# Kernel optimization log

Measured on AMD Instinct MI355X. Metric: run time of the kernel, lower is better.

Reference implementation:

```python
import jax, jax.numpy as jnp
import numpy as np

N = 256
DT = 1.0 / 4096.0
BATCH = 256
LENGTH = 4096

def _legt_transition(n):
    # HiPPO-LegT continuous-time transition (Gu et al.)
    Q = np.arange(n, dtype=np.float64)
    R = (2.0 * Q + 1.0) ** 0.5
    j, i = np.meshgrid(Q, Q)
    A = R[:, None] * np.where(i < j, (-1.0) ** (i - j), 1.0) * R[None, :]
    B = R[:, None]
    return -A, B

def _bilinear(A, B, dt):
    # scipy cont2discrete(method='bilinear'), alpha=0.5
    n = A.shape[0]
    ima = np.eye(n) - 0.5 * dt * A
    Ad = np.linalg.solve(ima, np.eye(n) + 0.5 * dt * A)
    Bd = np.linalg.solve(ima, dt * B)
    return Ad, Bd

def setup_inputs() -> dict:
    key = jax.random.key(0)
    Ac, Bc = _legt_transition(N)
    evals = (2.0 * np.arange(N, dtype=np.float64) + 1.0) ** 0.5
    C = evals @ Ac                        # (N,) readout from continuous A
    D = np.sum(evals * Bc.squeeze(-1))    # scalar
    scale = 1.0 / (1.0 - 0.5 * D * DT)
    C_discr = (scale * 0.5 * DT * C).astype(np.float32)          # (N,)
    D_discr = np.array([scale * (1.0 + 0.5 * DT * D)], np.float32)  # (1,)
    Ad, Bd = _bilinear(Ac, Bc, DT)
    inputs = jax.random.normal(key, (BATCH, LENGTH), dtype=jnp.float32)
    return {
        "inputs": inputs,
        "A": jnp.asarray(Ad, dtype=jnp.float32),
        "B": jnp.asarray(Bd.squeeze(-1), dtype=jnp.float32),
        "C_discr": jnp.asarray(C_discr),
        "D_discr": jnp.asarray(D_discr),
    }

def reference(inputs, A, B, C_discr, D_discr):
    # inputs: (batch, length). teacher_ratio=1.0 -> fully teacher-forced LTI scan:
    #   c_t = A c_{t-1} + B * u_t ;  pred_t = fac_t * (c_t @ C) + D * u_t
    # where fac_0 = 1 and fac_t = 2 for t > 0 (as in the torch loop).
    batch, length = inputs.shape
    c0 = jnp.zeros((batch, A.shape[0]), dtype=inputs.dtype)
    facs = jnp.where(jnp.arange(length) == 0, 1.0, 2.0).astype(inputs.dtype)

    def step(c, xs):
        x_t, fac = xs                                   # x_t: (batch,)
        c = c @ A.T + B[None, :] * x_t[:, None]         # (batch, N); F.linear(c, A)
        pred = fac * (c @ C_discr) + D_discr[0] * x_t   # (batch,)
        return c, pred

    _, preds = jax.lax.scan(step, c0, (inputs.T, facs))  # preds: (length, batch)
    return preds.T  # (batch, length)
```

## Files before the change

kernel.cpp:

```cpp
#include <hip/hip_runtime.h>


#define LENGTH 4096

#define WS_P2    0
#define WS_P4    65536
#define WS_P8    131072
#define WS_P16   196608
#define WS_P32   262144
#define WS_P64T  327680
#define WS_P128T 393216
#define WS_W     458752
#define WS_V     475136
#define WS_K     491520
#define WS_XH    495616
#define WS_XL    1019904
#define WS_AH    1544192
#define WS_AL    1609728

typedef __attribute__((ext_vector_type(8))) short bf16x8;
typedef __attribute__((ext_vector_type(4))) float f32x4;
#define MFMA(a, b, c) __builtin_amdgcn_mfma_f32_16x16x32_bf16(a, b, c, 0, 0, 0)

__device__ inline unsigned short f2bf(float f) {
    unsigned int u = __float_as_uint(f);
    return (unsigned short)((u + 0x7FFFu + ((u >> 16) & 1u)) >> 16);
}
__device__ inline void split2(float f, short& h, short& l) {
    unsigned short hu = f2bf(f);
    float fh = __uint_as_float((unsigned int)hu << 16);
    h = (short)hu;
    l = (short)f2bf(f - fh);
}

__global__ __launch_bounds__(1024) void mmrow(const float* __restrict__ X,
                                              const float* __restrict__ Y,
                                              float* __restrict__ Z) {
    const int i = blockIdx.x, t = threadIdx.x;
    const int j = t & 255, p = t >> 8;
    __shared__ float red[3][256];
    const float* xr = X + i * 256 + 64 * p;
    const float* yc = Y + (64 * p) * 256 + j;
    float a0 = 0.f, a1 = 0.f, a2 = 0.f, a3 = 0.f;
#pragma unroll
    for (int l = 0; l < 64; l += 4) {
        a0 = fmaf(xr[l + 0], yc[(l + 0) * 256], a0);
        a1 = fmaf(xr[l + 1], yc[(l + 1) * 256], a1);
        a2 = fmaf(xr[l + 2], yc[(l + 2) * 256], a2);
        a3 = fmaf(xr[l + 3], yc[(l + 3) * 256], a3);
    }
    float s = (a0 + a1) + (a2 + a3);
    if (p) red[p - 1][j] = s;
    __syncthreads();
    if (p == 0) Z[i * 256 + j] = s + red[0][j] + red[1][j] + red[2][j];
}

__global__ __launch_bounds__(1024) void mm2(const float* __restrict__ P32,
                                            float* __restrict__ P64T) {
    const int i = blockIdx.x, t = threadIdx.x;
    const int j = t & 255, p = t >> 8;
    __shared__ float red[3][256];
    const float* xr = P32 + i * 256 + 64 * p;
    const float* yc = P32 + (64 * p) * 256 + j;
    float a0 = 0.f, a1 = 0.f, a2 = 0.f, a3 = 0.f;
#pragma unroll
    for (int l = 0; l < 64; l += 4) {
        a0 = fmaf(xr[l + 0], yc[(l + 0) * 256], a0);
        a1 = fmaf(xr[l + 1], yc[(l + 1) * 256], a1);
        a2 = fmaf(xr[l + 2], yc[(l + 2) * 256], a2);
        a3 = fmaf(xr[l + 3], yc[(l + 3) * 256], a3);
    }
    float s = (a0 + a1) + (a2 + a3);
    if (p) red[p - 1][j] = s;
    __syncthreads();
    if (p == 0) P64T[j * 256 + i] = s + red[0][j] + red[1][j] + red[2][j];
}

__global__ __launch_bounds__(1024) void wvgen(const float* __restrict__ A,
                                              const float* __restrict__ B,
                                              const float* __restrict__ C,
                                              const float* __restrict__ P32,
                                              const float* __restrict__ P64T,
                                              const float* __restrict__ P128T,
                                              float* __restrict__ W,
                                              float* __restrict__ V) {
    const int t = threadIdx.x;
    const int bid = blockIdx.x;
    const int j = t & 255, p = t >> 8;
    __shared__ float cur[256];
    __shared__ float red[4][256];

    if (bid < 2) {
        float areg[64];
#pragma unroll
        for (int ii = 0; ii < 64; ++ii) areg[ii] = A[(64 * p + ii) * 256 + j];

        if (bid == 0) {
            if (t < 256) cur[t] = C[t];
            __syncthreads();
        } else {
            float s0 = 0.f, s1 = 0.f, s2 = 0.f, s3 = 0.f;
#pragma unroll 4
            for (int ii = 0; ii < 64; ii += 4) {
                s0 = fmaf(C[64 * p + ii + 0], P32[(64 * p + ii + 0) * 256 + j], s0);
                s1 = fmaf(C[64 * p + ii + 1], P32[(64 * p + ii + 1) * 256 + j], s1);
                s2 = fmaf(C[64 * p + ii + 2], P32[(64 * p + ii + 2) * 256 + j], s2);
                s3 = fmaf(C[64 * p + ii + 3], P32[(64 * p + ii + 3) * 256 + j], s3);
            }
            red[p][j] = (s0 + s1) + (s2 + s3);
            __syncthreads();
            if (p == 0) cur[j] = red[0][j] + red[1][j] + red[2][j] + red[3][j];
            __syncthreads();
        }
        const int base = bid * 32;
        if (p == 0) W[base * 256 + j] = cur[j];
        for (int r = 1; r < 32; ++r) {
            float s0 = 0.f, s1 = 0.f, s2 = 0.f, s3 = 0.f;
#pragma unroll
            for (int m = 0; m < 16; ++m) {
                float4 c4 = *reinterpret_cast<const float4*>(&cur[64 * p + 4 * m]);
                s0 = fmaf(c4.x, areg[4 * m + 0], s0);
                s1 = fmaf(c4.y, areg[4 * m + 1], s1);
                s2 = fmaf(c4.z, areg[4 * m + 2], s2);
                s3 = fmaf(c4.w, areg[4 * m + 3], s3);
            }
            red[p][j] = (s0 + s1) + (s2 + s3);
            __syncthreads();
            if (p == 0) {
                float s = red[0][j] + red[1][j] + red[2][j] + red[3][j];
                cur[j] = s;
                W[(base + r) * 256 + j] = s;
            }
            __syncthreads();
        }
    } else {
        const int i = j;
        float mreg[64];
#pragma unroll
        for (int jj = 0; jj < 64; ++jj) mreg[jj] = P128T[(64 * p + jj) * 256 + i];
        if (t < 256) cur[t] = B[t];
        __syncthreads();

        if (bid == 3) {
            float s0 = 0.f, s1 = 0.f, s2 = 0.f, s3 = 0.f;
#pragma unroll 4
            for (int jj = 0; jj < 64; jj += 4) {
                s0 = fmaf(P64T[(64 * p + jj + 0) * 256 + i], cur[64 * p + jj + 0], s0);
                s1 = fmaf(P64T[(64 * p + jj + 1) * 256 + i], cur[64 * p + jj + 1], s1);
                s2 = fmaf(P64T[(64 * p + jj + 2) * 256 + i], cur[64 * p + jj + 2], s2);
                s3 = fmaf(P64T[(64 * p + jj + 3) * 256 + i], cur[64 * p + jj + 3], s3);
            }
            red[p][i] = (s0 + s1) + (s2 + s3);
            __syncthreads();
            if (p == 0) cur[i] = red[0][i] + red[1][i] + red[2][i] + red[3][i];
            __syncthreads();
        }
        const int off = bid - 2;
        for (int m = 0; m < 32; ++m) {
            if (p == 0) V[(2 * m + off) * 256 + i] = cur[i];
            if (m == 31) break;
            float s0 = 0.f, s1 = 0.f, s2 = 0.f, s3 = 0.f;
#pragma unroll
            for (int mm = 0; mm < 16; ++mm) {
                float4 c4 = *reinterpret_cast<const float4*>(&cur[64 * p + 4 * mm]);
                s0 = fmaf(c4.x, mreg[4 * mm + 0], s0);
                s1 = fmaf(c4.y, mreg[4 * mm + 1], s1);
                s2 = fmaf(c4.z, mreg[4 * mm + 2], s2);
                s3 = fmaf(c4.w, mreg[4 * mm + 3], s3);
            }
            red[p][i] = (s0 + s1) + (s2 + s3);
            __syncthreads();
            if (p == 0) cur[i] = red[0][i] + red[1][i] + red[2][i] + red[3][i];
            __syncthreads();
        }
    }
}

__global__ __launch_bounds__(256) void kdot(const float* __restrict__ W,
                                            const float* __restrict__ V,
                                            float* __restrict__ K) {
    const int q = blockIdx.x, tid = threadIdx.x;
    const int r = tid & 63, p = tid >> 6;
    __shared__ float Wl[64 * 257];
    __shared__ float Vl[256];
    __shared__ float red[4][64];
    for (int u = 0; u < 64; ++u) Wl[u * 257 + tid] = W[u * 256 + tid];
    Vl[tid] = V[q * 256 + tid];
    __syncthreads();
    float s0 = 0.f, s1 = 0.f;
#pragma unroll
    for (int m = 0; m < 64; m += 2) {
        s0 = fmaf(Wl[r * 257 + 64 * p + m + 0], Vl[64 * p + m + 0], s0);
        s1 = fmaf(Wl[r * 257 + 64 * p + m + 1], Vl[64 * p + m + 1], s1);
    }
    red[p][r] = s0 + s1;
    __syncthreads();
    if (tid < 64) K[q * 64 + tid] = red[0][tid] + red[1][tid] + red[2][tid] + red[3][tid];
}

__global__ __launch_bounds__(256) void xsplit(const float* __restrict__ x,
                                              short* __restrict__ XH,
                                              short* __restrict__ XL) {
    const int w = threadIdx.x >> 6, lane = threadIdx.x & 63;
    const int p = blockIdx.x * 4 + w;
    const int c = p >> 4, blk = p & 15;
    const int b = blk * 16 + (lane & 15);
    const int s0 = c * 32 + 8 * (lane >> 4);
    const float4 v0 = reinterpret_cast<const float4*>(&x[b * LENGTH + s0])[0];
    const float4 v1 = reinterpret_cast<const float4*>(&x[b * LENGTH + s0])[1];
    const float f[8] = {v0.x, v0.y, v0.z, v0.w, v1.x, v1.y, v1.z, v1.w};
    bf16x8 hv, lv;
#pragma unroll
    for (int e = 0; e < 8; ++e) {
        short h, l;
        split2(f[e], h, l);
        hv[e] = h; lv[e] = l;
    }
    const int off = (p * 64 + lane) * 8;
    *reinterpret_cast<bf16x8*>(XH + off) = hv;
    *reinterpret_cast<bf16x8*>(XL + off) = lv;
}

__global__ __launch_bounds__(256) void afrag(const float* __restrict__ K,
                                             short* __restrict__ AH,
                                             short* __restrict__ AL) {
    const int m = blockIdx.x * 4 + (threadIdx.x >> 6);
    const int lane = threadIdx.x & 63;
    bf16x8 hv, lv;
#pragma unroll
    for (int e = 0; e < 8; ++e) {
        const int kidx = 16 * m + (lane & 15) - 8 * (lane >> 4) - e;
        const float kv = (kidx >= 0) ? K[kidx] : 0.f;
        short h, l;
        split2(kv, h, l);
        hv[e] = h; lv[e] = l;
    }
    const int off = (m * 64 + lane) * 8;
    *reinterpret_cast<bf16x8*>(AH + off) = hv;
    *reinterpret_cast<bf16x8*>(AL + off) = lv;
}

struct Frag {
    bf16x8 bh0, bh1, bl0, bl1;
    bf16x8 ah0, ah1, ah2, ah3, al0, al1, al2, al3;
    int d0, tile;
};

__global__ __launch_bounds__(512) void convm(const short* __restrict__ XH,
                                             const short* __restrict__ XL,
                                             const short* __restrict__ AH,
                                             const short* __restrict__ AL,
                                             const float* __restrict__ x,
                                             const float* __restrict__ Dp,
                                             float* __restrict__ out) {
    const int pr = blockIdx.x & 31;
    const int bt = blockIdx.x >> 5;
    const int tid = threadIdx.x;
    const int w = tid >> 6, lane = tid & 63;
    const int tA64 = pr * 64, tB64 = (63 - pr) * 64;
    const int nA = 2 * pr + 2;
    const int bt2 = bt * 2;

    __shared__ float lds[16 * 64 * 34];

    f32x4 acc[2][4][2];
#pragma unroll
    for (int t_ = 0; t_ < 2; ++t_)
#pragma unroll
        for (int r_ = 0; r_ < 4; ++r_)
#pragma unroll
            for (int c_ = 0; c_ < 2; ++c_) acc[t_][r_][c_] = f32x4{0.f, 0.f, 0.f, 0.f};

#define LOADF(F, IDX_) do {                                                    \
        const int i_ = (IDX_);                                                 \
        const int tl_ = (i_ < nA) ? 0 : 1;                                     \
        const int cc_ = i_ - (tl_ ? nA : 0);                                   \
        const int xo_ = ((cc_ * 16 + bt2) * 64 + lane) * 8;                    \
        F.bh0 = *reinterpret_cast<const bf16x8*>(XH + xo_);                    \
        F.bh1 = *reinterpret_cast<const bf16x8*>(XH + xo_ + 512);              \
        F.bl0 = *reinterpret_cast<const bf16x8*>(XL + xo_);                    \
        F.bl1 = *reinterpret_cast<const bf16x8*>(XL + xo_ + 512);              \
        const int d_ = (tl_ ? tB64 : tA64) - cc_ * 32;                         \
        F.d0 = d_; F.tile = tl_;                                               \
        const int m0_ = (d_ > 0 ? d_ : 0) >> 4;                                \
        const int m1_ = (d_ + 16 > 0 ? d_ + 16 : 0) >> 4;                      \
        const int m2_ = (d_ + 32 > 0 ? d_ + 32 : 0) >> 4;                      \
        const int m3_ = (d_ + 48 > 0 ? d_ + 48 : 0) >> 4;                      \
        F.ah0 = *reinterpret_cast<const bf16x8*>(AH + (m0_ * 64 + lane) * 8);  \
        F.al0 = *reinterpret_cast<const bf16x8*>(AL + (m0_ * 64 + lane) * 8);  \
        F.ah1 = *reinterpret_cast<const bf16x8*>(AH + (m1_ * 64 + lane) * 8);  \
        F.al1 = *reinterpret_cast<const bf16x8*>(AL + (m1_ * 64 + lane) * 8);  \
        F.ah2 = *reinterpret_cast<const bf16x8*>(AH + (m2_ * 64 + lane) * 8);  \
        F.al2 = *reinterpret_cast<const bf16x8*>(AL + (m2_ * 64 + lane) * 8);  \
        F.ah3 = *reinterpret_cast<const bf16x8*>(AH + (m3_ * 64 + lane) * 8);  \
        F.al3 = *reinterpret_cast<const bf16x8*>(AL + (m3_ * 64 + lane) * 8);  \
    } while (0)

#define ONER(F, T, R, AHF, ALF)                                                \
        if (F.d0 + 16 * R >= 0) {                                              \
            acc[T][R][0] = MFMA(F.AHF, F.bh0, acc[T][R][0]);                   \
            acc[T][R][1] = MFMA(F.AHF, F.bh1, acc[T][R][1]);                   \
            acc[T][R][0] = MFMA(F.AHF, F.bl0, acc[T][R][0]);                   \
            acc[T][R][1] = MFMA(F.AHF, F.bl1, acc[T][R][1]);                   \
            acc[T][R][0] = MFMA(F.ALF, F.bh0, acc[T][R][0]);                   \
            acc[T][R][1] = MFMA(F.ALF, F.bh1, acc[T][R][1]);                   \
        }

#define APPLY(F) do {                                                          \
        if (F.tile == 0) {                                                     \
            ONER(F, 0, 0, ah0, al0) ONER(F, 0, 1, ah1, al1)                    \
            ONER(F, 0, 2, ah2, al2) ONER(F, 0, 3, ah3, al3)                    \
        } else {                                                               \
            ONER(F, 1, 0, ah0, al0) ONER(F, 1, 1, ah1, al1)                    \
            ONER(F, 1, 2, ah2, al2) ONER(F, 1, 3, ah3, al3)                    \
        }                                                                      \
    } while (0)

    Frag f0, f1;
    LOADF(f0, w);
    int idx = w;
    while (true) {
        const int n1 = idx + 8;
        const bool h1 = n1 < 130;
        if (h1) LOADF(f1, n1);
        APPLY(f0);
        if (!h1) break;
        const int n2 = n1 + 8;
        const bool h2 = n2 < 130;
        if (h2) LOADF(f0, n2);
        APPLY(f1);
        if (!h2) break;
        idx = n2;
    }

    const int lq = lane >> 4, lr = lane & 15;
#pragma unroll
    for (int t_ = 0; t_ < 2; ++t_)
#pragma unroll
        for (int r_ = 0; r_ < 4; ++r_)
#pragma unroll
            for (int c_ = 0; c_ < 2; ++c_)
#pragma unroll
                for (int e_ = 0; e_ < 4; ++e_)
                    lds[((w * 2 + t_) * 64 + (r_ * 16 + lq * 4 + e_)) * 34 +
                        (c_ * 16 + lr)] = acc[t_][r_][c_][e_];
    __syncthreads();

    const float D = Dp[0];
    const int b = tid >> 4;
    const int t4 = (tid & 15) * 4;
#pragma unroll
    for (int t_ = 0; t_ < 2; ++t_) {
        const int tbase = t_ ? tB64 : tA64;
        float s0 = 0.f, s1 = 0.f, s2 = 0.f, s3 = 0.f;
#pragma unroll
        for (int w_ = 0; w_ < 8; ++w_) {
            const float* lp = &lds[((w_ * 2 + t_) * 64 + t4) * 34 + b];
            s0 += lp[0]; s1 += lp[34]; s2 += lp[68]; s3 += lp[102];
        }
        const int g = (bt * 32 + b) * LENGTH + tbase + t4;
        const float4 xv = *reinterpret_cast<const float4*>(x + g);
        float4 o;
        o.x = 2.f * s0 + D * xv.x;
        o.y = 2.f * s1 + D * xv.y;
        o.z = 2.f * s2 + D * xv.z;
        o.w = 2.f * s3 + D * xv.w;
        if (tbase == 0 && t4 == 0) o.x -= s0;
        *reinterpret_cast<float4*>(out + g) = o;
    }
}

extern "C" void kernel_launch(void* const* d_in, const int* in_sizes, int n_in,
                              void* d_out, int out_size, void* d_ws, size_t ws_size,
                              hipStream_t stream) {
    const float* x  = (const float*)d_in[0];
    const float* A  = (const float*)d_in[1];
    const float* B  = (const float*)d_in[2];
    const float* C  = (const float*)d_in[3];
    const float* Dp = (const float*)d_in[4];
    float* out = (float*)d_out;
    float* ws  = (float*)d_ws;

    float* P2    = ws + WS_P2;
    float* P4    = ws + WS_P4;
    float* P8    = ws + WS_P8;
    float* P16   = ws + WS_P16;
    float* P32   = ws + WS_P32;
    float* P64T  = ws + WS_P64T;
    float* P128T = ws + WS_P128T;
    float* Wm    = ws + WS_W;
    float* Vm    = ws + WS_V;
    float* K     = ws + WS_K;
    short* XHs   = (short*)(ws + WS_XH);
    short* XLs   = (short*)(ws + WS_XL);
    short* AHs   = (short*)(ws + WS_AH);
    short* ALs   = (short*)(ws + WS_AL);

    xsplit<<<512, 256, 0, stream>>>(x, XHs, XLs);
    mmrow<<<256, 1024, 0, stream>>>(A, A, P2);
    mmrow<<<256, 1024, 0, stream>>>(P2, P2, P4);
    mmrow<<<256, 1024, 0, stream>>>(P4, P4, P8);
    mmrow<<<256, 1024, 0, stream>>>(P8, P8, P16);
    mmrow<<<256, 1024, 0, stream>>>(P16, P16, P32);
    mm2<<<256, 1024, 0, stream>>>(P32, P64T);
    mmrow<<<256, 1024, 0, stream>>>(P64T, P64T, P128T);
    wvgen<<<4, 1024, 0, stream>>>(A, B, C, P32, P64T, P128T, Wm, Vm);
    kdot<<<64, 256, 0, stream>>>(Wm, Vm, K);
    afrag<<<64, 256, 0, stream>>>(K, AHs, ALs);
    convm<<<256, 512, 0, stream>>>(XHs, XLs, AHs, ALs, x, Dp, out);
}
```

Baseline: 103.8 us.

## Fuse setup kernels, parallelize W generation, merge K dot with fragment split

Merges the input bf16 split into the first squaring kernel and folds the W-row generation into the P128 squaring launch. W is now built by four blocks of 16 steps instead of two blocks of 32, which shortens the serial chain. The kdot and afrag kernels become one kfrag kernel that computes only the K values each block needs. convm replaces its strided double-buffered fragment loop with a contiguous per-wave chunk that reuses A fragments across steps. This cuts launch count and serial latency, at the cost of more complex index logic and some recomputed K entries.

Result: slower. 126.4 us (+21.7%).

```diff
diff --git a/kernel.cpp b/kernel.cpp
--- a/kernel.cpp
+++ b/kernel.cpp
@@ -12,11 +12,10 @@
 #define WS_P128T 393216
 #define WS_W     458752
 #define WS_V     475136
-#define WS_K     491520
-#define WS_XH    495616
-#define WS_XL    1019904
-#define WS_AH    1544192
-#define WS_AL    1609728
+#define WS_XH    491520
+#define WS_XL    1015808
+#define WS_AH    1540096
+#define WS_AL    1605632
 
 typedef __attribute__((ext_vector_type(8))) short bf16x8;
 typedef __attribute__((ext_vector_type(4))) float f32x4;
@@ -33,13 +32,12 @@
     l = (short)f2bf(f - fh);
 }
 
-__global__ __launch_bounds__(1024) void mmrow(const float* __restrict__ X,
-                                              const float* __restrict__ Y,
-                                              float* __restrict__ Z) {
-    const int i = blockIdx.x, t = threadIdx.x;
+__device__ __forceinline__ void mm_body(const float* __restrict__ X,
+                                        const float* __restrict__ Y,
+                                        float* __restrict__ Z,
+                                        int row, int t, bool trans, float* red) {
     const int j = t & 255, p = t >> 8;
-    __shared__ float red[3][256];
-    const float* xr = X + i * 256 + 64 * p;
+    const float* xr = X + row * 256 + 64 * p;
     const float* yc = Y + (64 * p) * 256 + j;
     float a0 = 0.f, a1 = 0.f, a2 = 0.f, a3 = 0.f;
 #pragma unroll
@@ -50,160 +48,29 @@
         a3 = fmaf(xr[l + 3], yc[(l + 3) * 256], a3);
     }
     float s = (a0 + a1) + (a2 + a3);
-    if (p) red[p - 1][j] = s;
+    if (p) red[(p - 1) * 256 + j] = s;
     __syncthreads();
-    if (p == 0) Z[i * 256 + j] = s + red[0][j] + red[1][j] + red[2][j];
-}
-
-__global__ __launch_bounds__(1024) void mm2(const float* __restrict__ P32,
-                                            float* __restrict__ P64T) {
-    const int i = blockIdx.x, t = threadIdx.x;
-    const int j = t & 255, p = t >> 8;
-    __shared__ float red[3][256];
-    const float* xr = P32 + i * 256 + 64 * p;
-    const float* yc = P32 + (64 * p) * 256 + j;
-    float a0 = 0.f, a1 = 0.f, a2 = 0.f, a3 = 0.f;
-#pragma unroll
-    for (int l = 0; l < 64; l += 4) {
-        a0 = fmaf(xr[l + 0], yc[(l + 0) * 256], a0);
-        a1 = fmaf(xr[l + 1], yc[(l + 1) * 256], a1);
-        a2 = fmaf(xr[l + 2], yc[(l + 2) * 256], a2);
-        a3 = fmaf(xr[l + 3], yc[(l + 3) * 256], a3);
-    }
-    float s = (a0 + a1) + (a2 + a3);
-    if (p) red[p - 1][j] = s;
-    __syncthreads();
-    if (p == 0) P64T[j * 256 + i] = s + red[0][j] + red[1][j] + red[2][j];
-}
-
-__global__ __launch_bounds__(1024) void wvgen(const float* __restrict__ A,
-                                              const float* __restrict__ B,
-                                              const float* __restrict__ C,
-                                              const float* __restrict__ P32,
-                                              const float* __restrict__ P64T,
-                                              const float* __restrict__ P128T,
-                                              float* __restrict__ W,
-                                              float* __restrict__ V) {
+    if (!p) {
+        float z = s + red[j] + red[256 + j] + red[512 + j];
+        if (trans) Z[j * 256 + row] = z;
+        else       Z[row * 256 + j] = z;
+    }
+}
+
+__global__ __launch_bounds__(1024) void fused0(const float* __restrict__ A,
+                                               const float* __restrict__ x,
+                                               float* __restrict__ P2,
+                                               short* __restrict__ XH,
+                                               short* __restrict__ XL) {
+    __shared__ float red[3 * 256];
     const int t = threadIdx.x;
-    const int bid = blockIdx.x;
-    const int j = t & 255, p = t >> 8;
-    __shared__ float cur[256];
-    __shared__ float red[4][256];
-
-    if (bid < 2) {
-        float areg[64];
-#pragma unroll
-        for (int ii = 0; ii < 64; ++ii) areg[ii] = A[(64 * p + ii) * 256 + j];
-
-        if (bid == 0) {
-            if (t < 256) cur[t] = C[t];
-            __syncthreads();
-        } else {
-            float s0 = 0.f, s1 = 0.f, s2 = 0.f, s3 = 0.f;
-#pragma unroll 4
-            for (int ii = 0; ii < 64; ii += 4) {
-                s0 = fmaf(C[64 * p + ii + 0], P32[(64 * p + ii + 0) * 256 + j], s0);
-                s1 = fmaf(C[64 * p + ii + 1], P32[(64 * p + ii + 1) * 256 + j], s1);
-                s2 = fmaf(C[64 * p + ii + 2], P32[(64 * p + ii + 2) * 256 + j], s2);
-                s3 = fmaf(C[64 * p + ii + 3], P32[(64 * p + ii + 3) * 256 + j], s3);
-            }
-            red[p][j] = (s0 + s1) + (s2 + s3);
-            __syncthreads();
-            if (p == 0) cur[j] = red[0][j] + red[1][j] + red[2][j] + red[3][j];
-            __syncthreads();
-        }
-        const int base = bid * 32;
-        if (p == 0) W[base * 256 + j] = cur[j];
-        for (int r = 1; r < 32; ++r) {
-            float s0 = 0.f, s1 = 0.f, s2 = 0.f, s3 = 0.f;
-#pragma unroll
-            for (int m = 0; m < 16; ++m) {
-                float4 c4 = *reinterpret_cast<const float4*>(&cur[64 * p + 4 * m]);
-                s0 = fmaf(c4.x, areg[4 * m + 0], s0);
-                s1 = fmaf(c4.y, areg[4 * m + 1], s1);
-                s2 = fmaf(c4.z, areg[4 * m + 2], s2);
-                s3 = fmaf(c4.w, areg[4 * m + 3], s3);
-            }
-            red[p][j] = (s0 + s1) + (s2 + s3);
-            __syncthreads();
-            if (p == 0) {
-                float s = red[0][j] + red[1][j] + red[2][j] + red[3][j];
-                cur[j] = s;
-                W[(base + r) * 256 + j] = s;
-            }
-            __syncthreads();
-        }
-    } else {
-        const int i = j;
-        float mreg[64];
-#pragma unroll
-        for (int jj = 0; jj < 64; ++jj) mreg[jj] = P128T[(64 * p + jj) * 256 + i];
-        if (t < 256) cur[t] = B[t];
-        __syncthreads();
-
-        if (bid == 3) {
-            float s0 = 0.f, s1 = 0.f, s2 = 0.f, s3 = 0.f;
-#pragma unroll 4
-            for (int jj = 0; jj < 64; jj += 4) {
-                s0 = fmaf(P64T[(64 * p + jj + 0) * 256 + i], cur[64 * p + jj + 0], s0);
-                s1 = fmaf(P64T[(64 * p + jj + 1) * 256 + i], cur[64 * p + jj + 1], s1);
-                s2 = fmaf(P64T[(64 * p + jj + 2) * 256 + i], cur[64 * p + jj + 2], s2);
-                s3 = fmaf(P64T[(64 * p + jj + 3) * 256 + i], cur[64 * p + jj + 3], s3);
-            }
-            red[p][i] = (s0 + s1) + (s2 + s3);
-            __syncthreads();
-            if (p == 0) cur[i] = red[0][i] + red[1][i] + red[2][i] + red[3][i];
-            __syncthreads();
-        }
-        const int off = bid - 2;
-        for (int m = 0; m < 32; ++m) {
-            if (p == 0) V[(2 * m + off) * 256 + i] = cur[i];
-            if (m == 31) break;
-            float s0 = 0.f, s1 = 0.f, s2 = 0.f, s3 = 0.f;
-#pragma unroll
-            for (int mm = 0; mm < 16; ++mm) {
-                float4 c4 = *reinterpret_cast<const float4*>(&cur[64 * p + 4 * mm]);
-                s0 = fmaf(c4.x, mreg[4 * mm + 0], s0);
-                s1 = fmaf(c4.y, mreg[4 * mm + 1], s1);
-                s2 = fmaf(c4.z, mreg[4 * mm + 2], s2);
-                s3 = fmaf(c4.w, mreg[4 * mm + 3], s3);
-            }
-            red[p][i] = (s0 + s1) + (s2 + s3);
-            __syncthreads();
-            if (p == 0) cur[i] = red[0][i] + red[1][i] + red[2][i] + red[3][i];
-            __syncthreads();
-        }
-    }
-}
-
-__global__ __launch_bounds__(256) void kdot(const float* __restrict__ W,
-                                            const float* __restrict__ V,
-                                            float* __restrict__ K) {
-    const int q = blockIdx.x, tid = threadIdx.x;
-    const int r = tid & 63, p = tid >> 6;
-    __shared__ float Wl[64 * 257];
-    __shared__ float Vl[256];
-    __shared__ float red[4][64];
-    for (int u = 0; u < 64; ++u) Wl[u * 257 + tid] = W[u * 256 + tid];
-    Vl[tid] = V[q * 256 + tid];
-    __syncthreads();
-    float s0 = 0.f, s1 = 0.f;
-#pragma unroll
-    for (int m = 0; m < 64; m += 2) {
-        s0 = fmaf(Wl[r * 257 + 64 * p + m + 0], Vl[64 * p + m + 0], s0);
-        s1 = fmaf(Wl[r * 257 + 64 * p + m + 1], Vl[64 * p + m + 1], s1);
-    }
-    red[p][r] = s0 + s1;
-    __syncthreads();
-    if (tid < 64) K[q * 64 + tid] = red[0][tid] + red[1][tid] + red[2][tid] + red[3][tid];
-}
-
-__global__ __launch_bounds__(256) void xsplit(const float* __restrict__ x,
-                                              short* __restrict__ XH,
-                                              short* __restrict__ XL) {
-    const int w = threadIdx.x >> 6, lane = threadIdx.x & 63;
-    const int p = blockIdx.x * 4 + w;
-    const int c = p >> 4, blk = p & 15;
+    if (blockIdx.x < 256) {
+        mm_body(A, A, P2, blockIdx.x, t, false, red);
+        return;
+    }
+    const int wv = t >> 6, lane = t & 63;
+    const int pj = (blockIdx.x - 256) * 16 + wv;
+    const int c = pj >> 4, blk = pj & 15;
     const int b = blk * 16 + (lane & 15);
     const int s0 = c * 32 + 8 * (lane >> 4);
     const float4 v0 = reinterpret_cast<const float4*>(&x[b * LENGTH + s0])[0];
@@ -216,35 +83,220 @@
         split2(f[e], h, l);
         hv[e] = h; lv[e] = l;
     }
-    const int off = (p * 64 + lane) * 8;
+    const int off = (pj * 64 + lane) * 8;
     *reinterpret_cast<bf16x8*>(XH + off) = hv;
     *reinterpret_cast<bf16x8*>(XL + off) = lv;
 }
 
-__global__ __launch_bounds__(256) void afrag(const float* __restrict__ K,
+__global__ __launch_bounds__(1024) void mmsq(const float* __restrict__ S,
+                                             float* __restrict__ D) {
+    __shared__ float red[3 * 256];
+    mm_body(S, S, D, blockIdx.x, threadIdx.x, false, red);
+}
+__global__ __launch_bounds__(1024) void mmsqT(const float* __restrict__ S,
+                                              float* __restrict__ D) {
+    __shared__ float red[3 * 256];
+    mm_body(S, S, D, blockIdx.x, threadIdx.x, true, red);
+}
+
+__global__ __launch_bounds__(1024) void p128w(const float* __restrict__ P64T,
+                                              float* __restrict__ P128T,
+                                              const float* __restrict__ A,
+                                              const float* __restrict__ C,
+                                              const float* __restrict__ P16,
+                                              const float* __restrict__ P32,
+                                              float* __restrict__ W) {
+    __shared__ float red[3 * 256];
+    __shared__ float cur[256];
+    __shared__ float red4[4][256];
+    const int t = threadIdx.x;
+    if (blockIdx.x < 256) {
+        mm_body(P64T, P64T, P128T, blockIdx.x, t, false, red);
+        return;
+    }
+    const int c = blockIdx.x - 256;
+    const int j = t & 255, p = t >> 8;
+    float areg[64];
+#pragma unroll
+    for (int ii = 0; ii < 64; ++ii) areg[ii] = A[(64 * p + ii) * 256 + j];
+
+    if (c == 0) {
+        if (t < 256) cur[t] = C[t];
+        __syncthreads();
+    } else {
+        const float* M1 = (c == 2) ? P32 : P16;
+        float s0 = 0.f, s1 = 0.f;
+#pragma unroll
+        for (int ii = 0; ii < 64; ii += 2) {
+            s0 = fmaf(C[64 * p + ii],     M1[(64 * p + ii) * 256 + j],     s0);
+            s1 = fmaf(C[64 * p + ii + 1], M1[(64 * p + ii + 1) * 256 + j], s1);
+        }
+        red4[p][j] = s0 + s1;
+        __syncthreads();
+        if (!p) cur[j] = red4[0][j] + red4[1][j] + red4[2][j] + red4[3][j];
+        __syncthreads();
+        if (c == 3) {
+            float q0 = 0.f, q1 = 0.f;
+#pragma unroll
+            for (int ii = 0; ii < 64; ii += 2) {
+                q0 = fmaf(cur[64 * p + ii],     P32[(64 * p + ii) * 256 + j],     q0);
+                q1 = fmaf(cur[64 * p + ii + 1], P32[(64 * p + ii + 1) * 256 + j], q1);
+            }
+            red4[p][j] = q0 + q1;
+            __syncthreads();
+            if (!p) cur[j] = red4[0][j] + red4[1][j] + red4[2][j] + red4[3][j];
+            __syncthreads();
+        }
+    }
+    for (int s_ = 0; s_ < 16; ++s_) {
+        if (!p) W[(16 * c + s_) * 256 + j] = cur[j];
+        if (s_ == 15) break;
+        float s0 = 0.f, s1 = 0.f;
+#pragma unroll
+        for (int m = 0; m < 16; ++m) {
+            float4 c4 = *reinterpret_cast<const float4*>(&cur[64 * p + 4 * m]);
+            s0 = fmaf(c4.x, areg[4 * m + 0], s0);
+            s1 = fmaf(c4.y, areg[4 * m + 1], s1);
+            s0 = fmaf(c4.z, areg[4 * m + 2], s0);
+            s1 = fmaf(c4.w, areg[4 * m + 3], s1);
+        }
+        red4[p][j] = s0 + s1;
+        __syncthreads();
+        if (!p) cur[j] = red4[0][j] + red4[1][j] + red4[2][j] + red4[3][j];
+        __syncthreads();
+    }
+}
+
+__global__ __launch_bounds__(1024) void vgen(const float* __restrict__ P64T,
+                                             const float* __restrict__ P128T,
+                                             const float* __restrict__ B,
+                                             float* __restrict__ V) {
+    __shared__ float cur[256];
+    __shared__ float red4[4][256];
+    const int t = threadIdx.x;
+    const int i = t & 255, p = t >> 8;
+    const int c = blockIdx.x;
+    float mreg[64];
+#pragma unroll
+    for (int jj = 0; jj < 64; ++jj) mreg[jj] = P128T[(64 * p + jj) * 256 + i];
+
+    if (c == 0) {
+        if (t < 256) cur[t] = B[t];
+        __syncthreads();
+    } else {
+        float s0 = 0.f, s1 = 0.f;
+#pragma unroll
+        for (int jj = 0; jj < 64; jj += 2) {
+            s0 = fmaf(P64T[(64 * p + jj) * 256 + i],     B[64 * p + jj],     s0);
+            s1 = fmaf(P64T[(64 * p + jj + 1) * 256 + i], B[64 * p + jj + 1], s1);
+        }
+        red4[p][i] = s0 + s1;
+        __syncthreads();
+        if (!p) cur[i] = red4[0][i] + red4[1][i] + red4[2][i] + red4[3][i];
+        __syncthreads();
+    }
+    for (int s_ = 0; s_ < 32; ++s_) {
+        if (!p) V[(2 * s_ + c) * 256 + i] = cur[i];
+        if (s_ == 31) break;
+        float s0 = 0.f, s1 = 0.f;
+#pragma unroll
+        for (int m = 0; m < 16; ++m) {
+            float4 c4 = *reinterpret_cast<const float4*>(&cur[64 * p + 4 * m]);
+            s0 = fmaf(c4.x, mreg[4 * m + 0], s0);
+            s1 = fmaf(c4.y, mreg[4 * m + 1], s1);
+            s0 = fmaf(c4.z, mreg[4 * m + 2], s0);
+            s1 = fmaf(c4.w, mreg[4 * m + 3], s1);
+        }
+        red4[p][i] = s0 + s1;
+        __syncthreads();
+        if (!p) cur[i] = red4[0][i] + red4[1][i] + red4[2][i] + red4[3][i];
+        __syncthreads();
+    }
+}
+
+__global__ __launch_bounds__(256) void kfrag(const float* __restrict__ Wm,
+                                             const float* __restrict__ Vm,
                                              short* __restrict__ AH,
                                              short* __restrict__ AL) {
-    const int m = blockIdx.x * 4 + (threadIdx.x >> 6);
-    const int lane = threadIdx.x & 63;
-    bf16x8 hv, lv;
-#pragma unroll
-    for (int e = 0; e < 8; ++e) {
-        const int kidx = 16 * m + (lane & 15) - 8 * (lane >> 4) - e;
-        const float kv = (kidx >= 0) ? K[kidx] : 0.f;
-        short h, l;
-        split2(kv, h, l);
-        hv[e] = h; lv[e] = l;
-    }
-    const int off = (m * 64 + lane) * 8;
-    *reinterpret_cast<bf16x8*>(AH + off) = hv;
-    *reinterpret_cast<bf16x8*>(AL + off) = lv;
-}
-
-struct Frag {
-    bf16x8 bh0, bh1, bl0, bl1;
-    bf16x8 ah0, ah1, ah2, ah3, al0, al1, al2, al3;
-    int d0, tile;
-};
+    const int bid = blockIdx.x, t = threadIdx.x;
+    __shared__ float Wl[64 * 257];
+    __shared__ float Vl[3 * 256];
+    __shared__ float kl[144];
+    for (int r = 0; r < 64; ++r) Wl[r * 257 + t] = Wm[r * 256 + t];
+#pragma unroll
+    for (int qq = 0; qq < 3; ++qq) {
+        const int q = 2 * bid - 1 + qq;
+        Vl[qq * 256 + t] = (q >= 0) ? Vm[q * 256 + t] : 0.f;
+    }
+    __syncthreads();
+    if (t < 143) {
+        const int tau = 128 * bid - 15 + t;
+        float s = 0.f;
+        if (tau >= 0) {
+            const int r = tau & 63;
+            const int qq = (tau >> 6) - (2 * bid - 1);
+            const float* wr = &Wl[r * 257];
+            const float* vr = &Vl[qq * 256];
+            float s0 = 0.f, s1 = 0.f, s2 = 0.f, s3 = 0.f;
+#pragma unroll 16
+            for (int i = 0; i < 256; i += 4) {
+                s0 = fmaf(wr[i + 0], vr[i + 0], s0);
+                s1 = fmaf(wr[i + 1], vr[i + 1], s1);
+                s2 = fmaf(wr[i + 2], vr[i + 2], s2);
+                s3 = fmaf(wr[i + 3], vr[i + 3], s3);
+            }
+            s = (s0 + s1) + (s2 + s3);
+        }
+        kl[t] = s;
+    }
+    __syncthreads();
+    const int wv = t >> 6, lane = t & 63;
+#pragma unroll
+    for (int e2 = 0; e2 < 2; ++e2) {
+        const int ep = 2 * wv + e2;
+        const int m = 8 * bid + ep;
+        bf16x8 hv, lv;
+#pragma unroll
+        for (int el = 0; el < 8; ++el) {
+            const int rel = 16 * ep + (lane & 15) - 8 * (lane >> 4) - el + 15;
+            short h, l;
+            split2(kl[rel], h, l);
+            hv[el] = h; lv[el] = l;
+        }
+        const int off = (m * 64 + lane) * 8;
+        *reinterpret_cast<bf16x8*>(AH + off) = hv;
+        *reinterpret_cast<bf16x8*>(AL + off) = lv;
+    }
+}
+
+#define AHP(M_) (*reinterpret_cast<const bf16x8*>(AH + ((M_) * 64 + lane) * 8))
+#define ALP(M_) (*reinterpret_cast<const bf16x8*>(AL + ((M_) * 64 + lane) * 8))
+#define XHP(O_) (*reinterpret_cast<const bf16x8*>(XH + (O_)))
+#define XLP(O_) (*reinterpret_cast<const bf16x8*>(XL + (O_)))
+
+#define ONER6(AHF, ALF, T, R)                                   \
+    acc[T][R][0] = MFMA(AHF, bh0, acc[T][R][0]);                \
+    acc[T][R][1] = MFMA(AHF, bh1, acc[T][R][1]);                \
+    acc[T][R][0] = MFMA(AHF, bl0, acc[T][R][0]);                \
+    acc[T][R][1] = MFMA(AHF, bl1, acc[T][R][1]);                \
+    acc[T][R][0] = MFMA(ALF, bh0, acc[T][R][0]);                \
+    acc[T][R][1] = MFMA(ALF, bh1, acc[T][R][1]);
+
+#define APPLYT(T)                                               \
+    { if (d >= 0)      { ONER6(ah0, al0, T, 0) }                \
+      if (d + 16 >= 0) { ONER6(ah1, al1, T, 1) }                \
+      if (d + 32 >= 0) { ONER6(ah2, al2, T, 2) }                \
+      if (d + 48 >= 0) { ONER6(ah3, al3, T, 3) } }
+
+#define LOADA_FULL(D_)                                          \
+    { const int m0_ = ((D_) > 0 ? (D_) : 0) >> 4;               \
+      const int m1_ = ((D_) + 16 > 0 ? (D_) + 16 : 0) >> 4;     \
+      const int m2_ = ((D_) + 32 > 0 ? (D_) + 32 : 0) >> 4;     \
+      const int m3_ = ((D_) + 48 > 0 ? (D_) + 48 : 0) >> 4;     \
+      ah0 = AHP(m0_); al0 = ALP(m0_);                           \
+      ah1 = AHP(m1_); al1 = ALP(m1_);                           \
+      ah2 = AHP(m2_); al2 = ALP(m2_);                           \
+      ah3 = AHP(m3_); al3 = ALP(m3_); }
 
 __global__ __launch_bounds__(512) void convm(const short* __restrict__ XH,
                                              const short* __restrict__ XL,
@@ -260,7 +312,6 @@
     const int tA64 = pr * 64, tB64 = (63 - pr) * 64;
     const int nA = 2 * pr + 2;
     const int bt2 = bt * 2;
-
     __shared__ float lds[16 * 64 * 34];
 
     f32x4 acc[2][4][2];
@@ -271,66 +322,51 @@
 #pragma unroll
             for (int c_ = 0; c_ < 2; ++c_) acc[t_][r_][c_] = f32x4{0.f, 0.f, 0.f, 0.f};
 
-#define LOADF(F, IDX_) do {                                                    \
-        const int i_ = (IDX_);                                                 \
-        const int tl_ = (i_ < nA) ? 0 : 1;                                     \
-        const int cc_ = i_ - (tl_ ? nA : 0);                                   \
-        const int xo_ = ((cc_ * 16 + bt2) * 64 + lane) * 8;                    \
-        F.bh0 = *reinterpret_cast<const bf16x8*>(XH + xo_);                    \
-        F.bh1 = *reinterpret_cast<const bf16x8*>(XH + xo_ + 512);              \
-        F.bl0 = *reinterpret_cast<const bf16x8*>(XL + xo_);                    \
-        F.bl1 = *reinterpret_cast<const bf16x8*>(XL + xo_ + 512);              \
-        const int d_ = (tl_ ? tB64 : tA64) - cc_ * 32;                         \
-        F.d0 = d_; F.tile = tl_;                                               \
-        const int m0_ = (d_ > 0 ? d_ : 0) >> 4;                                \
-        const int m1_ = (d_ + 16 > 0 ? d_ + 16 : 0) >> 4;                      \
-        const int m2_ = (d_ + 32 > 0 ? d_ + 32 : 0) >> 4;                      \
-        const int m3_ = (d_ + 48 > 0 ? d_ + 48 : 0) >> 4;                      \
-        F.ah0 = *reinterpret_cast<const bf16x8*>(AH + (m0_ * 64 + lane) * 8);  \
-        F.al0 = *reinterpret_cast<const bf16x8*>(AL + (m0_ * 64 + lane) * 8);  \
-        F.ah1 = *reinterpret_cast<const bf16x8*>(AH + (m1_ * 64 + lane) * 8);  \
-        F.al1 = *reinterpret_cast<const bf16x8*>(AL + (m1_ * 64 + lane) * 8);  \
-        F.ah2 = *reinterpret_cast<const bf16x8*>(AH + (m2_ * 64 + lane) * 8);  \
-        F.al2 = *reinterpret_cast<const bf16x8*>(AL + (m2_ * 64 + lane) * 8);  \
-        F.ah3 = *reinterpret_cast<const bf16x8*>(AH + (m3_ * 64 + lane) * 8);  \
-        F.al3 = *reinterpret_cast<const bf16x8*>(AL + (m3_ * 64 + lane) * 8);  \
-    } while (0)
-
-#define ONER(F, T, R, AHF, ALF)                                                \
-        if (F.d0 + 16 * R >= 0) {                                              \
-            acc[T][R][0] = MFMA(F.AHF, F.bh0, acc[T][R][0]);                   \
-            acc[T][R][1] = MFMA(F.AHF, F.bh1, acc[T][R][1]);                   \
-            acc[T][R][0] = MFMA(F.AHF, F.bl0, acc[T][R][0]);                   \
-            acc[T][R][1] = MFMA(F.AHF, F.bl1, acc[T][R][1]);                   \
-            acc[T][R][0] = MFMA(F.ALF, F.bh0, acc[T][R][0]);                   \
-            acc[T][R][1] = MFMA(F.ALF, F.bh1, acc[T][R][1]);                   \
-        }
-
-#define APPLY(F) do {                                                          \
-        if (F.tile == 0) {                                                     \
-            ONER(F, 0, 0, ah0, al0) ONER(F, 0, 1, ah1, al1)                    \
-            ONER(F, 0, 2, ah2, al2) ONER(F, 0, 3, ah3, al3)                    \
-        } else {                                                               \
-            ONER(F, 1, 0, ah0, al0) ONER(F, 1, 1, ah1, al1)                    \
-            ONER(F, 1, 2, ah2, al2) ONER(F, 1, 3, ah3, al3)                    \
-        }                                                                      \
-    } while (0)
-
-    Frag f0, f1;
-    LOADF(f0, w);
-    int idx = w;
+    const int lo = (130 * w) >> 3, hi = (130 * (w + 1)) >> 3;
+
+    bf16x8 ah0, ah1, ah2, ah3, al0, al1, al2, al3, bh0, bh1, bl0, bl1;
+    int idx = lo;
+    int tile = (idx < nA) ? 0 : 1;
+    int cc = idx - (tile ? nA : 0);
+    int d = (tile ? tB64 : tA64) - 32 * cc;
+    LOADA_FULL(d);
+    {
+        const int xo = ((cc * 16 + bt2) * 64 + lane) * 8;
+        bh0 = XHP(xo); bh1 = XHP(xo + 512);
+        bl0 = XLP(xo); bl1 = XLP(xo + 512);
+    }
+
     while (true) {
-        const int n1 = idx + 8;
-        const bool h1 = n1 < 130;
-        if (h1) LOADF(f1, n1);
-        APPLY(f0);
-        if (!h1) break;
-        const int n2 = n1 + 8;
-        const bool h2 = n2 < 130;
-        if (h2) LOADF(f0, n2);
-        APPLY(f1);
-        if (!h2) break;
-        idx = n2;
+        const int nxt = idx + 1;
+        const bool hn = nxt < hi;
+        bf16x8 tbh0, tbh1, tbl0, tbl1, tah0, tah1, tal0, tal1;
+        int tilen = tile, dn = d;
+        bool sw = false;
+        if (hn) {
+            tilen = (nxt < nA) ? 0 : 1;
+            const int ccn = nxt - (tilen ? nA : 0);
+            dn = (tilen ? tB64 : tA64) - 32 * ccn;
+            sw = (tilen != tile);
+            const int xo = ((ccn * 16 + bt2) * 64 + lane) * 8;
+            tbh0 = XHP(xo); tbh1 = XHP(xo + 512);
+            tbl0 = XLP(xo); tbl1 = XLP(xo + 512);
+            if (!sw) {
+                const int n0 = (dn > 0 ? dn : 0) >> 4;
+                const int n1 = (dn + 16 > 0 ? dn + 16 : 0) >> 4;
+                tah0 = AHP(n0); tal0 = ALP(n0);
+                tah1 = AHP(n1); tal1 = ALP(n1);
+            }
+        }
+        if (tile == 0) { APPLYT(0) } else { APPLYT(1) }
+        if (!hn) break;
+        if (!sw) {
+            ah3 = ah1; ah2 = ah0; al3 = al1; al2 = al0;
+            ah0 = tah0; ah1 = tah1; al0 = tal0; al1 = tal1;
+        } else {
+            LOADA_FULL(dn);
+        }
+        bh0 = tbh0; bh1 = tbh1; bl0 = tbl0; bl1 = tbl1;
+        tile = tilen; d = dn; idx = nxt;
     }
 
     const int lq = lane >> 4, lr = lane & 15;
@@ -390,22 +426,19 @@
     float* P128T = ws + WS_P128T;
     float* Wm    = ws + WS_W;
     float* Vm    = ws + WS_V;
-    float* K     = ws + WS_K;
     short* XHs   = (short*)(ws + WS_XH);
     short* XLs   = (short*)(ws + WS_XL);
     short* AHs   = (short*)(ws + WS_AH);
     short* ALs   = (short*)(ws + WS_AL);
 
-    xsplit<<<512, 256, 0, stream>>>(x, XHs, XLs);
-    mmrow<<<256, 1024, 0, stream>>>(A, A, P2);
-    mmrow<<<256, 1024, 0, stream>>>(P2, P2, P4);
-    mmrow<<<256, 1024, 0, stream>>>(P4, P4, P8);
-    mmrow<<<256, 1024, 0, stream>>>(P8, P8, P16);
-    mmrow<<<256, 1024, 0, stream>>>(P16, P16, P32);
-    mm2<<<256, 1024, 0, stream>>>(P32, P64T);
-    mmrow<<<256, 1024, 0, stream>>>(P64T, P64T, P128T);
-    wvgen<<<4, 1024, 0, stream>>>(A, B, C, P32, P64T, P128T, Wm, Vm);
-    kdot<<<64, 256, 0, stream>>>(Wm, Vm, K);
-    afrag<<<64, 256, 0, stream>>>(K, AHs, ALs);
+    fused0<<<384, 1024, 0, stream>>>(A, x, P2, XHs, XLs);
+    mmsq<<<256, 1024, 0, stream>>>(P2, P4);
+    mmsq<<<256, 1024, 0, stream>>>(P4, P8);
+    mmsq<<<256, 1024, 0, stream>>>(P8, P16);
+    mmsq<<<256, 1024, 0, stream>>>(P16, P32);
+    mmsqT<<<256, 1024, 0, stream>>>(P32, P64T);
+    p128w<<<260, 1024, 0, stream>>>(P64T, P128T, A, C, P16, P32, Wm);
+    vgen<<<2, 1024, 0, stream>>>(P64T, P128T, B, Vm);
+    kfrag<<<32, 256, 0, stream>>>(Wm, Vm, AHs, ALs);
     convm<<<256, 512, 0, stream>>>(XHs, XLs, AHs, ALs, x, Dp, out);
 }
```
